# Performance work log

Hardware: AMD Instinct MI355X
Metric: run time of the kernel (lower is better)

## Reference

```python
import jax, jax.numpy as jnp
import numpy as np

OBS_RADIUS = 1.0
N = 8192      # num_agents
IN_DIM = 4    # state dim: [x, y, vx, vy]
HID = 64


def setup_inputs() -> dict:
    key = jax.random.key(0)
    ks = jax.random.split(key, 6)
    states = jax.random.normal(ks[0], (N, IN_DIM), dtype=jnp.float32)
    W1 = jax.random.normal(ks[1], (IN_DIM, HID), dtype=jnp.float32) / np.sqrt(IN_DIM).astype(np.float32)
    b1 = jnp.zeros((HID,), jnp.float32)
    W2 = jax.random.normal(ks[2], (HID, HID), dtype=jnp.float32) / np.sqrt(HID).astype(np.float32)
    b2 = jnp.zeros((HID,), jnp.float32)
    cw = jax.random.normal(ks[3], (HID,), dtype=jnp.float32) / np.sqrt(HID).astype(np.float32)  # Conv1d(64,1,1) weight
    cb = jnp.zeros((1,), jnp.float32)
    return {"states": states, "W1": W1, "b1": b1, "W2": W2, "b2": b2, "cw": cw, "cb": cb}


def _build_norm_adj(states):
    # radius graph on first two coords (positions); no self edges in the edge list,
    # GCNConv then adds self-loops and does symmetric D^-1/2 (A+I) D^-1/2 normalization.
    pos = states[:, :2]
    d2 = jnp.sum((pos[:, None, :] - pos[None, :, :]) ** 2, axis=-1)  # [N, N]
    mask = d2 <= jnp.asarray(OBS_RADIUS ** 2, states.dtype)          # [N, N] bool (incl. diagonal)
    eye = jnp.eye(N, dtype=bool)
    A_hat = jnp.where(mask & ~eye, jnp.asarray(1.0, states.dtype), 0.0) + jnp.eye(N, dtype=states.dtype)
    dinv = jax.lax.rsqrt(jnp.sum(A_hat, axis=1))                     # deg >= 1 (self loop)
    A_norm = dinv[:, None] * A_hat * dinv[None, :]
    return A_norm, mask


def reference(states, W1, b1, W2, b2, cw, cb):
    A_norm, mask = _build_norm_adj(states)
    # GCNConv 1: aggregate(normalized adj) of X W, plus bias, ReLU
    h = jax.nn.relu(A_norm @ (states @ W1) + b1)   # [N, 64]
    # GCNConv 2
    h = jax.nn.relu(A_norm @ (h @ W2) + b2)        # [N, 64]
    # Conv1d(64 -> 1, kernel=1): pointwise linear over channels
    out = h @ cw[:, None] + cb                     # [N, 1]
    return out, mask
```

## Files before the change

kernel.cpp:

```cpp
#include <hip/hip_runtime.h>
#include <hip/hip_bf16.h>
#include <stdint.h>

#define NPTS 8192
#define KSPLIT 8

typedef float f32x4 __attribute__((ext_vector_type(4)));
typedef short s16x8 __attribute__((ext_vector_type(8)));

__device__ __forceinline__ unsigned short f2bf(float f) {
    unsigned int u = __builtin_bit_cast(unsigned int, f);
    u += 0x7FFFu + ((u >> 16) & 1u);
    return (unsigned short)(u >> 16);
}


__global__ __launch_bounds__(256) void k_mask(const float* __restrict__ states,
                                              float* __restrict__ mout,
                                              unsigned long long* __restrict__ maskb,
                                              float* __restrict__ dinv) {
    __shared__ float2 xy[NPTS];
    int tid = threadIdx.x;
    for (int r = tid; r < NPTS; r += 256) {
        float4 s = ((const float4*)states)[r];
        xy[r] = make_float2(s.x, s.y);
    }
    __syncthreads();
    int wv = tid >> 6, L = tid & 63;
    int rowbase = blockIdx.x * 16 + wv * 4;
    for (int rr = 0; rr < 4; ++rr) {
        int i = rowbase + rr;
        float2 pi = xy[i];
        int deg = 0;
        float* orow = mout + (size_t)i * NPTS;
        unsigned long long* brow = maskb + (size_t)i * 128;
        for (int it = 0; it < 128; ++it) {
            int j = it * 64 + L;
            float2 pj = xy[j];
            float dx = pi.x - pj.x;
            float dy = pi.y - pj.y;
            float d2 = __fadd_rn(__fmul_rn(dx, dx), __fmul_rn(dy, dy));
            bool pred = (d2 <= 1.0f);
            __builtin_nontemporal_store(pred ? 1.0f : 0.0f, &orow[j]);
            unsigned long long b = __ballot(pred);
            if (L == 0) brow[it] = b;
            deg += (int)__popcll(b);
        }
        if (L == 0) dinv[i] = rsqrtf((float)deg);
    }
}

__global__ __launch_bounds__(256) void k_y1(const float* __restrict__ states,
                                            const float* __restrict__ W1,
                                            const float* __restrict__ dinv,
                                            uint4* __restrict__ y) {
    int gid = blockIdx.x * 256 + threadIdx.x;
    int L = gid & 63, ct = (gid >> 6) & 3, kb = gid >> 8;
    int n = L & 15, quad = L >> 4;
    int col = ct * 16 + n;
    float w0 = W1[col], w1 = W1[64 + col], w2 = W1[128 + col], w3 = W1[192 + col];
    unsigned short frag[8];
#pragma unroll
    for (int t = 0; t < 8; ++t) {
        int k = kb * 32 + quad * 8 + t;
        float4 s = ((const float4*)states)[k];
        float acc = s.x * w0 + s.y * w1 + s.z * w2 + s.w * w3;
        frag[t] = f2bf(dinv[k] * acc);
    }
    uint4 u;
    u.x = (unsigned)frag[0] | ((unsigned)frag[1] << 16);
    u.y = (unsigned)frag[2] | ((unsigned)frag[3] << 16);
    u.z = (unsigned)frag[4] | ((unsigned)frag[5] << 16);
    u.w = (unsigned)frag[6] | ((unsigned)frag[7] << 16);
    y[gid] = u;
}

__global__ __launch_bounds__(256) void k_agg(const uint4* __restrict__ y,
                                             const unsigned int* __restrict__ maskb,
                                             float* __restrict__ zp) {
    int tid = threadIdx.x;
    int wv = tid >> 6, L = tid & 63;
    int bid = blockIdx.x;
    int mt = bid >> 3, ks = bid & (KSPLIT - 1);
    int n = L & 15, quad = L >> 4;
    int i0 = mt * 128 + wv * 32 + n;
    const unsigned int* mrow0 = maskb + (size_t)i0 * 256 + ks * 32;
    const unsigned int* mrow1 = mrow0 + 16 * 256;
    const uint4* yb = y + (size_t)(ks * 32) * 256 + L;

    f32x4 acc[2][4] = {{{0,0,0,0},{0,0,0,0},{0,0,0,0},{0,0,0,0}},
                       {{0,0,0,0},{0,0,0,0},{0,0,0,0},{0,0,0,0}}};
    uint4 bcur[4];
    unsigned int mw0 = mrow0[0], mw1 = mrow1[0];
#pragma unroll
    for (int ct = 0; ct < 4; ++ct) bcur[ct] = yb[ct * 64];

    for (int kb = 0; kb < 32; ++kb) {
        uint4 bnext[4]; unsigned int mwn0 = 0, mwn1 = 0;
        if (kb < 31) {
            const uint4* p = yb + (kb + 1) * 256;
#pragma unroll
            for (int ct = 0; ct < 4; ++ct) bnext[ct] = p[ct * 64];
            mwn0 = mrow0[kb + 1];
            mwn1 = mrow1[kb + 1];
        }
        unsigned int byte0 = (mw0 >> (quad * 8)) & 0xFFu;
        unsigned int byte1 = (mw1 >> (quad * 8)) & 0xFFu;
        s16x8 a0, a1;
#pragma unroll
        for (int t = 0; t < 8; ++t) {
            a0[t] = (short)(((byte0 >> t) & 1u) ? 0x3F80 : 0);
            a1[t] = (short)(((byte1 >> t) & 1u) ? 0x3F80 : 0);
        }
#pragma unroll
        for (int ct = 0; ct < 4; ++ct) {
            s16x8 b = __builtin_bit_cast(s16x8, bcur[ct]);
            acc[0][ct] = __builtin_amdgcn_mfma_f32_16x16x32_bf16(a0, b, acc[0][ct], 0, 0, 0);
            acc[1][ct] = __builtin_amdgcn_mfma_f32_16x16x32_bf16(a1, b, acc[1][ct], 0, 0, 0);
        }
#pragma unroll
        for (int ct = 0; ct < 4; ++ct) bcur[ct] = bnext[ct];
        mw0 = mwn0; mw1 = mwn1;
    }
    float* zb = zp + (size_t)ks * (NPTS * 64) + (size_t)(mt * 128 + wv * 32) * 64;
#pragma unroll
    for (int g = 0; g < 2; ++g)
#pragma unroll
        for (int ct = 0; ct < 4; ++ct)
#pragma unroll
            for (int r = 0; r < 4; ++r)
                zb[(g * 16 + quad * 4 + r) * 64 + ct * 16 + n] = acc[g][ct][r];
}

__global__ __launch_bounds__(256) void k_h1y2(const float* __restrict__ zp,
                                              const float* __restrict__ dinv,
                                              const float* __restrict__ b1,
                                              const float* __restrict__ W2,
                                              uint4* __restrict__ y2) {
    __shared__ float w2s[4096];
    __shared__ float hbuf[8 * 64];
    __shared__ unsigned short ybuf[8 * 64];
    int tid = threadIdx.x;
#pragma unroll
    for (int s = 0; s < 16; ++s) w2s[s * 256 + tid] = W2[s * 256 + tid];
    int j0 = blockIdx.x * 8;
#pragma unroll
    for (int e = tid; e < 512; e += 256) {
        int r = e >> 6, c = e & 63;
        int j = j0 + r;
        float z = 0.0f;
#pragma unroll
        for (int s = 0; s < KSPLIT; ++s) z += zp[(size_t)s * (NPTS * 64) + j * 64 + c];
        hbuf[r * 64 + c] = fmaxf(dinv[j] * z + b1[c], 0.0f);
    }
    __syncthreads();
#pragma unroll
    for (int e = tid; e < 512; e += 256) {
        int r = e >> 6, c = e & 63;
        const float* hr = hbuf + r * 64;
        float acc = 0.0f;
#pragma unroll
        for (int m = 0; m < 64; ++m) acc = fmaf(hr[m], w2s[m * 64 + c], acc);
        ybuf[r * 64 + c] = f2bf(dinv[j0 + r] * acc);
    }
    __syncthreads();
    if (tid < 64) {
        int c = tid;
        unsigned short v[8];
#pragma unroll
        for (int r = 0; r < 8; ++r) v[r] = ybuf[r * 64 + c];
        uint4 u;
        u.x = (unsigned)v[0] | ((unsigned)v[1] << 16);
        u.y = (unsigned)v[2] | ((unsigned)v[3] << 16);
        u.z = (unsigned)v[4] | ((unsigned)v[5] << 16);
        u.w = (unsigned)v[6] | ((unsigned)v[7] << 16);
        int kb = j0 >> 5, quad = (j0 >> 3) & 3, ct = c >> 4, nn = c & 15;
        y2[(kb * 4 + ct) * 64 + quad * 16 + nn] = u;
    }
}

__global__ __launch_bounds__(256) void k_out(const float* __restrict__ zp,
                                             const float* __restrict__ dinv,
                                             const float* __restrict__ b2,
                                             const float* __restrict__ cw,
                                             const float* __restrict__ cb,
                                             float* __restrict__ out) {
    int tid = threadIdx.x;
    int wv = tid >> 6, L = tid & 63;
    int i = blockIdx.x * 4 + wv;
    int idx = i * 64 + L;
    float z = 0.0f;
#pragma unroll
    for (int s = 0; s < KSPLIT; ++s) z += zp[(size_t)s * (NPTS * 64) + idx];
    float h = fmaxf(dinv[i] * z + b2[L], 0.0f);
    float v = h * cw[L];
#pragma unroll
    for (int off = 32; off > 0; off >>= 1) v += __shfl_down(v, off, 64);
    if (L == 0) out[i] = v + cb[0];
}

extern "C" void kernel_launch(void* const* d_in, const int* in_sizes, int n_in,
                              void* d_out, int out_size, void* d_ws, size_t ws_size,
                              hipStream_t stream) {
    const float* states = (const float*)d_in[0];
    const float* W1 = (const float*)d_in[1];
    const float* b1 = (const float*)d_in[2];
    const float* W2 = (const float*)d_in[3];
    const float* b2 = (const float*)d_in[4];
    const float* cw = (const float*)d_in[5];
    const float* cb = (const float*)d_in[6];
    float* out = (float*)d_out;
    float* mout = out + NPTS;

    char* ws = (char*)d_ws;
    float* dinv               = (float*)(ws);
    unsigned long long* maskb = (unsigned long long*)(ws + (1 << 16));
    uint4* y1                 = (uint4*)(ws + (1 << 16) + (8 << 20));
    uint4* y2                 = (uint4*)(ws + (1 << 16) + (9 << 20));
    float* zp                 = (float*)(ws + (1 << 16) + (10 << 20));

    hipLaunchKernelGGL(k_mask, dim3(512), dim3(256), 0, stream, states, mout, maskb, dinv);
    hipLaunchKernelGGL(k_y1,   dim3(256), dim3(256), 0, stream, states, W1, dinv, y1);
    hipLaunchKernelGGL(k_agg,  dim3(64 * KSPLIT), dim3(256), 0, stream,
                       y1, (const unsigned int*)maskb, zp);
    hipLaunchKernelGGL(k_h1y2, dim3(1024), dim3(256), 0, stream, zp, dinv, b1, W2, y2);
    hipLaunchKernelGGL(k_agg,  dim3(64 * KSPLIT), dim3(256), 0, stream,
                       y2, (const unsigned int*)maskb, zp);
    hipLaunchKernelGGL(k_out,  dim3(2048), dim3(256), 0, stream, zp, dinv, b2, cw, cb, out);
}
```

Baseline: 370.8 us.

## Fuse y1 into mask kernel, interleave mask rows, widen aggregation tiles

The k_y1 kernel is folded into k_mask. Each block computes its 16 rows' degree scaling in shared memory and writes the bf16 y1 fragments directly, which removes one launch and the dinv round trip through global memory. The mask loop now processes four rows per j-iteration using split x/y shared arrays, so each loaded neighbour position is reused four times and there is more independent work per load. The aggregation kernel now computes 64 rows per wave (four MFMA row groups) with KSPLIT raised to 16. Each y fragment is reused more, but the doubled number of fp32 partial sums makes the zp buffer larger, adds reduction work in the downstream kernels, and raises register pressure.

```diff
diff --git a/kernel.cpp b/kernel.cpp
--- a/kernel.cpp
+++ b/kernel.cpp
@@ -3,7 +3,7 @@
 #include <stdint.h>
 
 #define NPTS 8192
-#define KSPLIT 8
+#define KSPLIT 16
 
 typedef float f32x4 __attribute__((ext_vector_type(4)));
 typedef short s16x8 __attribute__((ext_vector_type(8)));
@@ -16,63 +16,75 @@
 
 
 __global__ __launch_bounds__(256) void k_mask(const float* __restrict__ states,
+                                              const float* __restrict__ W1,
                                               float* __restrict__ mout,
                                               unsigned long long* __restrict__ maskb,
-                                              float* __restrict__ dinv) {
-    __shared__ float2 xy[NPTS];
+                                              float* __restrict__ dinv,
+                                              uint4* __restrict__ y1) {
+    __shared__ float xs[NPTS];
+    __shared__ float ys[NPTS];
+    __shared__ float dls[16];
     int tid = threadIdx.x;
     for (int r = tid; r < NPTS; r += 256) {
         float4 s = ((const float4*)states)[r];
-        xy[r] = make_float2(s.x, s.y);
+        xs[r] = s.x; ys[r] = s.y;
     }
     __syncthreads();
     int wv = tid >> 6, L = tid & 63;
     int rowbase = blockIdx.x * 16 + wv * 4;
-    for (int rr = 0; rr < 4; ++rr) {
-        int i = rowbase + rr;
-        float2 pi = xy[i];
-        int deg = 0;
-        float* orow = mout + (size_t)i * NPTS;
-        unsigned long long* brow = maskb + (size_t)i * 128;
-        for (int it = 0; it < 128; ++it) {
-            int j = it * 64 + L;
-            float2 pj = xy[j];
-            float dx = pi.x - pj.x;
-            float dy = pi.y - pj.y;
+    float xi[4], yi[4];
+    int deg[4] = {0, 0, 0, 0};
+#pragma unroll
+    for (int rr = 0; rr < 4; ++rr) { xi[rr] = xs[rowbase + rr]; yi[rr] = ys[rowbase + rr]; }
+    for (int it = 0; it < 128; ++it) {
+        int j = it * 64 + L;
+        float xj = xs[j], yj = ys[j];
+#pragma unroll
+        for (int rr = 0; rr < 4; ++rr) {
+            float dx = xi[rr] - xj;
+            float dy = yi[rr] - yj;
             float d2 = __fadd_rn(__fmul_rn(dx, dx), __fmul_rn(dy, dy));
             bool pred = (d2 <= 1.0f);
-            __builtin_nontemporal_store(pred ? 1.0f : 0.0f, &orow[j]);
+            __builtin_nontemporal_store(pred ? 1.0f : 0.0f,
+                                        &mout[(size_t)(rowbase + rr) * NPTS + j]);
             unsigned long long b = __ballot(pred);
-            if (L == 0) brow[it] = b;
-            deg += (int)__popcll(b);
-        }
-        if (L == 0) dinv[i] = rsqrtf((float)deg);
-    }
-}
-
-__global__ __launch_bounds__(256) void k_y1(const float* __restrict__ states,
-                                            const float* __restrict__ W1,
-                                            const float* __restrict__ dinv,
-                                            uint4* __restrict__ y) {
-    int gid = blockIdx.x * 256 + threadIdx.x;
-    int L = gid & 63, ct = (gid >> 6) & 3, kb = gid >> 8;
-    int n = L & 15, quad = L >> 4;
-    int col = ct * 16 + n;
-    float w0 = W1[col], w1 = W1[64 + col], w2 = W1[128 + col], w3 = W1[192 + col];
-    unsigned short frag[8];
-#pragma unroll
-    for (int t = 0; t < 8; ++t) {
-        int k = kb * 32 + quad * 8 + t;
-        float4 s = ((const float4*)states)[k];
-        float acc = s.x * w0 + s.y * w1 + s.z * w2 + s.w * w3;
-        frag[t] = f2bf(dinv[k] * acc);
-    }
-    uint4 u;
-    u.x = (unsigned)frag[0] | ((unsigned)frag[1] << 16);
-    u.y = (unsigned)frag[2] | ((unsigned)frag[3] << 16);
-    u.z = (unsigned)frag[4] | ((unsigned)frag[5] << 16);
-    u.w = (unsigned)frag[6] | ((unsigned)frag[7] << 16);
-    y[gid] = u;
+            if (L == 0) maskb[(size_t)(rowbase + rr) * 128 + it] = b;
+            deg[rr] += (int)__popcll(b);
+        }
+    }
+    if (L == 0) {
+#pragma unroll
+        for (int rr = 0; rr < 4; ++rr) {
+            float dv = rsqrtf((float)deg[rr]);
+            dinv[rowbase + rr] = dv;
+            dls[wv * 4 + rr] = dv;
+        }
+    }
+    __syncthreads();
+    if (tid < 128) {
+        int ql = tid >> 6;
+        int ct = (tid >> 4) & 3;
+        int nn = tid & 15;
+        int col = ct * 16 + nn;
+        float w0 = W1[col], w1 = W1[64 + col], w2 = W1[128 + col], w3 = W1[192 + col];
+        unsigned short frag[8];
+#pragma unroll
+        for (int t = 0; t < 8; ++t) {
+            int rloc = ql * 8 + t;
+            int k = blockIdx.x * 16 + rloc;
+            float4 s = ((const float4*)states)[k];
+            float acc = s.x * w0 + s.y * w1 + s.z * w2 + s.w * w3;
+            frag[t] = f2bf(dls[rloc] * acc);
+        }
+        uint4 u;
+        u.x = (unsigned)frag[0] | ((unsigned)frag[1] << 16);
+        u.y = (unsigned)frag[2] | ((unsigned)frag[3] << 16);
+        u.z = (unsigned)frag[4] | ((unsigned)frag[5] << 16);
+        u.w = (unsigned)frag[6] | ((unsigned)frag[7] << 16);
+        int kb = blockIdx.x >> 1;
+        int quad = ql + 2 * (blockIdx.x & 1);
+        y1[(kb * 4 + ct) * 64 + quad * 16 + nn] = u;
+    }
 }
 
 __global__ __launch_bounds__(256) void k_agg(const uint4* __restrict__ y,
@@ -80,51 +92,61 @@
                                              float* __restrict__ zp) {
     int tid = threadIdx.x;
     int wv = tid >> 6, L = tid & 63;
-    int bid = blockIdx.x;
-    int mt = bid >> 3, ks = bid & (KSPLIT - 1);
+    int mt = blockIdx.x >> 4, ks = blockIdx.x & (KSPLIT - 1);
     int n = L & 15, quad = L >> 4;
-    int i0 = mt * 128 + wv * 32 + n;
-    const unsigned int* mrow0 = maskb + (size_t)i0 * 256 + ks * 32;
+    int i0 = mt * 256 + wv * 64 + n;
+    const unsigned int* mrow0 = maskb + (size_t)i0 * 256 + ks * 16;
     const unsigned int* mrow1 = mrow0 + 16 * 256;
-    const uint4* yb = y + (size_t)(ks * 32) * 256 + L;
-
-    f32x4 acc[2][4] = {{{0,0,0,0},{0,0,0,0},{0,0,0,0},{0,0,0,0}},
+    const unsigned int* mrow2 = mrow0 + 32 * 256;
+    const unsigned int* mrow3 = mrow0 + 48 * 256;
+    const uint4* yb = y + (size_t)(ks * 16) * 256 + L;
+
+    f32x4 acc[4][4] = {{{0,0,0,0},{0,0,0,0},{0,0,0,0},{0,0,0,0}},
+                       {{0,0,0,0},{0,0,0,0},{0,0,0,0},{0,0,0,0}},
+                       {{0,0,0,0},{0,0,0,0},{0,0,0,0},{0,0,0,0}},
                        {{0,0,0,0},{0,0,0,0},{0,0,0,0},{0,0,0,0}}};
     uint4 bcur[4];
-    unsigned int mw0 = mrow0[0], mw1 = mrow1[0];
+    unsigned int mw0 = mrow0[0], mw1 = mrow1[0], mw2 = mrow2[0], mw3 = mrow3[0];
 #pragma unroll
     for (int ct = 0; ct < 4; ++ct) bcur[ct] = yb[ct * 64];
 
-    for (int kb = 0; kb < 32; ++kb) {
-        uint4 bnext[4]; unsigned int mwn0 = 0, mwn1 = 0;
-        if (kb < 31) {
+    for (int kb = 0; kb < 16; ++kb) {
+        uint4 bnext[4];
+        unsigned int mwn0 = 0, mwn1 = 0, mwn2 = 0, mwn3 = 0;
+        if (kb < 15) {
             const uint4* p = yb + (kb + 1) * 256;
 #pragma unroll
             for (int ct = 0; ct < 4; ++ct) bnext[ct] = p[ct * 64];
-            mwn0 = mrow0[kb + 1];
-            mwn1 = mrow1[kb + 1];
-        }
-        unsigned int byte0 = (mw0 >> (quad * 8)) & 0xFFu;
-        unsigned int byte1 = (mw1 >> (quad * 8)) & 0xFFu;
-        s16x8 a0, a1;
+            mwn0 = mrow0[kb + 1]; mwn1 = mrow1[kb + 1];
+            mwn2 = mrow2[kb + 1]; mwn3 = mrow3[kb + 1];
+        }
+        unsigned int by0 = (mw0 >> (quad * 8)) & 0xFFu;
+        unsigned int by1 = (mw1 >> (quad * 8)) & 0xFFu;
+        unsigned int by2 = (mw2 >> (quad * 8)) & 0xFFu;
+        unsigned int by3 = (mw3 >> (quad * 8)) & 0xFFu;
+        s16x8 a0, a1, a2, a3;
 #pragma unroll
         for (int t = 0; t < 8; ++t) {
-            a0[t] = (short)(((byte0 >> t) & 1u) ? 0x3F80 : 0);
-            a1[t] = (short)(((byte1 >> t) & 1u) ? 0x3F80 : 0);
+            a0[t] = (short)(((by0 >> t) & 1u) ? 0x3F80 : 0);
+            a1[t] = (short)(((by1 >> t) & 1u) ? 0x3F80 : 0);
+            a2[t] = (short)(((by2 >> t) & 1u) ? 0x3F80 : 0);
+            a3[t] = (short)(((by3 >> t) & 1u) ? 0x3F80 : 0);
         }
 #pragma unroll
         for (int ct = 0; ct < 4; ++ct) {
             s16x8 b = __builtin_bit_cast(s16x8, bcur[ct]);
             acc[0][ct] = __builtin_amdgcn_mfma_f32_16x16x32_bf16(a0, b, acc[0][ct], 0, 0, 0);
             acc[1][ct] = __builtin_amdgcn_mfma_f32_16x16x32_bf16(a1, b, acc[1][ct], 0, 0, 0);
+            acc[2][ct] = __builtin_amdgcn_mfma_f32_16x16x32_bf16(a2, b, acc[2][ct], 0, 0, 0);
+            acc[3][ct] = __builtin_amdgcn_mfma_f32_16x16x32_bf16(a3, b, acc[3][ct], 0, 0, 0);
         }
 #pragma unroll
         for (int ct = 0; ct < 4; ++ct) bcur[ct] = bnext[ct];
-        mw0 = mwn0; mw1 = mwn1;
-    }
-    float* zb = zp + (size_t)ks * (NPTS * 64) + (size_t)(mt * 128 + wv * 32) * 64;
-#pragma unroll
-    for (int g = 0; g < 2; ++g)
+        mw0 = mwn0; mw1 = mwn1; mw2 = mwn2; mw3 = mwn3;
+    }
+    float* zb = zp + (size_t)ks * (NPTS * 64) + (size_t)(mt * 256 + wv * 64) * 64;
+#pragma unroll
+    for (int g = 0; g < 4; ++g)
 #pragma unroll
         for (int ct = 0; ct < 4; ++ct)
 #pragma unroll
@@ -219,12 +241,12 @@
     uint4* y2                 = (uint4*)(ws + (1 << 16) + (9 << 20));
     float* zp                 = (float*)(ws + (1 << 16) + (10 << 20));
 
-    hipLaunchKernelGGL(k_mask, dim3(512), dim3(256), 0, stream, states, mout, maskb, dinv);
-    hipLaunchKernelGGL(k_y1,   dim3(256), dim3(256), 0, stream, states, W1, dinv, y1);
-    hipLaunchKernelGGL(k_agg,  dim3(64 * KSPLIT), dim3(256), 0, stream,
+    hipLaunchKernelGGL(k_mask, dim3(512), dim3(256), 0, stream,
+                       states, W1, mout, maskb, dinv, y1);
+    hipLaunchKernelGGL(k_agg,  dim3(32 * KSPLIT), dim3(256), 0, stream,
                        y1, (const unsigned int*)maskb, zp);
     hipLaunchKernelGGL(k_h1y2, dim3(1024), dim3(256), 0, stream, zp, dinv, b1, W2, y2);
-    hipLaunchKernelGGL(k_agg,  dim3(64 * KSPLIT), dim3(256), 0, stream,
+    hipLaunchKernelGGL(k_agg,  dim3(32 * KSPLIT), dim3(256), 0, stream,
                        y2, (const unsigned int*)maskb, zp);
     hipLaunchKernelGGL(k_out,  dim3(2048), dim3(256), 0, stream, zp, dinv, b2, cw, cb, out);
 }
```

After: 373.6 us. About the same (+0.8%).
